# Performance work log

Hardware: AMD Instinct MI355X
Metric: run time of the kernel (lower is better)

The kernel has to match this reference:

```python
import jax, jax.numpy as jnp
import numpy as np

N_NODES = 100000
N_EDGES = 1600000
D_FEAT = 128
HIDDEN = 256


def setup_inputs() -> dict:
    key = jax.random.key(0)
    k1, k2, k3, k4, k5, k6, k7 = jax.random.split(key, 7)
    h = jax.random.normal(k1, (N_NODES, D_FEAT), dtype=jnp.float32)
    src = jax.random.randint(k2, (N_EDGES,), 0, N_NODES, dtype=jnp.int64)
    dst = jax.random.randint(k3, (N_EDGES,), 0, N_NODES, dtype=jnp.int64)
    # Linear weights, torch layout: W [out, in], b [out]
    lim1 = 1.0 / np.sqrt(2 * D_FEAT)
    W1_w = jax.random.uniform(k4, (HIDDEN, 2 * D_FEAT), minval=-lim1, maxval=lim1, dtype=jnp.float32)
    W1_b = jax.random.uniform(k5, (HIDDEN,), minval=-lim1, maxval=lim1, dtype=jnp.float32)
    lim2 = 1.0 / np.sqrt(HIDDEN)
    W2_w = jax.random.uniform(k6, (1, HIDDEN), minval=-lim2, maxval=lim2, dtype=jnp.float32)
    W2_b = jax.random.uniform(k7, (1,), minval=-lim2, maxval=lim2, dtype=jnp.float32)
    return {"h": h, "src": src, "dst": dst, "W1_w": W1_w, "W1_b": W1_b, "W2_w": W2_w, "W2_b": W2_b}


def reference(h, src, dst, W1_w, W1_b, W2_w, W2_b):
    # gather per-edge src/dst node features and concat: [E, 2D]
    x = jnp.concatenate([h[src], h[dst]], axis=1)
    # Linear -> ReLU -> Linear, squeeze last dim -> [E]
    hid = jax.nn.relu(x @ W1_w.T + W1_b)          # [E, H]
    score = (hid @ W2_w.T + W2_b)[:, 0]           # [E]
    return score
```

## Files before the change

kernel.cpp:

```cpp
#include <hip/hip_runtime.h>


#define NNODES 100000
#define E_TOTAL 1600000
#define D 128
#define K2 256
#define H 256

#define TILE_M 32
#define NTILES (E_TOTAL / TILE_M)
#define GRID 2500

typedef short bf16x8 __attribute__((ext_vector_type(8)));
typedef float f32x4 __attribute__((ext_vector_type(4)));
typedef const __attribute__((address_space(1))) unsigned short* gas_t;
typedef __attribute__((address_space(3))) unsigned short* las_t;

#if defined(__has_attribute)
#if __has_attribute(amdgpu_waves_per_eu)
#define LB __launch_bounds__(256) __attribute__((amdgpu_waves_per_eu(2, 2)))
#else
#define LB __launch_bounds__(256, 2)
#endif
#else
#define LB __launch_bounds__(256, 2)
#endif

__device__ __forceinline__ unsigned short f2bf(float f) {
    unsigned u = __float_as_uint(f);
    u += 0x7fff + ((u >> 16) & 1);
    return (unsigned short)(u >> 16);
}

__global__ void cvt_kernel(const float* __restrict__ h, const float* __restrict__ w1,
                           unsigned short* __restrict__ hbf, unsigned short* __restrict__ w1bf,
                           int n4h, int n4w) {
    int i = blockIdx.x * blockDim.x + threadIdx.x;
    const float* s; unsigned short* d; int j;
    if (i < n4h) { s = h; d = hbf; j = i; }
    else if (i < n4h + n4w) { s = w1; d = w1bf; j = i - n4h; }
    else return;
    float4 v = ((const float4*)s)[j];
    ushort4 o;
    o.x = f2bf(v.x); o.y = f2bf(v.y); o.z = f2bf(v.z); o.w = f2bf(v.w);
    ((ushort4*)d)[j] = o;
}

__global__ LB void edge_mlp(
    const unsigned short* __restrict__ hbf,
    const int* __restrict__ srcE,
    const int* __restrict__ dstE,
    const unsigned short* __restrict__ w1bf,
    const float* __restrict__ b1,
    const float* __restrict__ w2,
    const float* __restrict__ b2p,
    float* __restrict__ out)
{
    __shared__ __align__(16) unsigned short X[2][TILE_M * K2];
    __shared__ float red[2][TILE_M][5];

    const int tid = threadIdx.x;
    const int wave = tid >> 6;
    const int lane = tid & 63;
    const int lane15 = lane & 15;
    const int quad = lane >> 4;

    bf16x8 B[8][4];
#pragma unroll
    for (int kit = 0; kit < 8; ++kit) {
#pragma unroll
        for (int nt = 0; nt < 4; ++nt) {
            int n = wave * 64 + nt * 16 + lane15;
            int k = kit * 32 + quad * 8;
            B[kit][nt] = *(const bf16x8*)(w1bf + n * K2 + k);
        }
    }

    float b1v[4], w2v[4];
#pragma unroll
    for (int nt = 0; nt < 4; ++nt) {
        int n = wave * 64 + nt * 16 + lane15;
        b1v[nt] = b1[n];
        w2v[nt] = w2[n];
    }
    const float b2 = *b2p;

    const int r_off = tid >> 5;
    const int c = (tid & 31) ^ (r_off & 7);
    const int half = c >> 4;
    const int fc = c & 15;
    const int* idx_base = half ? dstE : srcE;
    const int gshort = fc * 8;

    const int t0 = blockIdx.x;
    int inode[4];

#pragma unroll
    for (int it = 0; it < 4; ++it)
        inode[it] = idx_base[t0 * TILE_M + it * 8 + r_off];
#pragma unroll
    for (int it = 0; it < 4; ++it)
        __builtin_amdgcn_global_load_lds(
            (gas_t)(hbf + inode[it] * D + gshort),
            (las_t)(&X[0][0] + it * 2048 + wave * 512), 16, 0, 0);
    {
        const int t1 = t0 + GRID;
#pragma unroll
        for (int it = 0; it < 4; ++it)
            inode[it] = idx_base[t1 * TILE_M + it * 8 + r_off];
    }

    int buf = 0;
    int prev_eb = -1;

    for (int tile = t0; tile < NTILES; tile += GRID) {
        __syncthreads();

        const int nt1 = tile + GRID;
        if (nt1 < NTILES) {
            unsigned short* Xn = &X[buf ^ 1][0];
#pragma unroll
            for (int it = 0; it < 4; ++it)
                __builtin_amdgcn_global_load_lds(
                    (gas_t)(hbf + inode[it] * D + gshort),
                    (las_t)(Xn + it * 2048 + wave * 512), 16, 0, 0);
        }
        const int nt2 = tile + 2 * GRID;
        if (nt2 < NTILES) {
            const int eb2 = nt2 * TILE_M;
#pragma unroll
            for (int it = 0; it < 4; ++it)
                inode[it] = idx_base[eb2 + it * 8 + r_off];
        }
        if (prev_eb >= 0 && tid < TILE_M) {
            float s = b2;
#pragma unroll
            for (int w = 0; w < 4; ++w) s += red[buf ^ 1][tid][w];
            out[prev_eb + tid] = s;
        }

        const unsigned short* Xc = &X[buf][0];
        f32x4 acc[2][4];
        const f32x4 zero = {0.f, 0.f, 0.f, 0.f};
#pragma unroll
        for (int ms = 0; ms < 2; ++ms)
#pragma unroll
            for (int nt = 0; nt < 4; ++nt)
                acc[ms][nt] = zero;

#pragma unroll
        for (int kit = 0; kit < 8; ++kit) {
            const int p8 = (((kit * 4 + quad) ^ (lane15 & 7))) * 8;
            bf16x8 a[2];
#pragma unroll
            for (int ms = 0; ms < 2; ++ms)
                a[ms] = *(const bf16x8*)&Xc[(ms * 16 + lane15) * K2 + p8];
#pragma unroll
            for (int ms = 0; ms < 2; ++ms)
#pragma unroll
                for (int nt = 0; nt < 4; ++nt)
                    acc[ms][nt] = __builtin_amdgcn_mfma_f32_16x16x32_bf16(
                        a[ms], B[kit][nt], acc[ms][nt], 0, 0, 0);
        }

#pragma unroll
        for (int ms = 0; ms < 2; ++ms) {
#pragma unroll
            for (int r = 0; r < 4; ++r) {
                float p = 0.f;
#pragma unroll
                for (int nt = 0; nt < 4; ++nt) {
                    float hv = acc[ms][nt][r] + b1v[nt];
                    p = fmaf(fmaxf(hv, 0.f), w2v[nt], p);
                }
                p += __shfl_xor(p, 1, 16);
                p += __shfl_xor(p, 2, 16);
                p += __shfl_xor(p, 4, 16);
                p += __shfl_xor(p, 8, 16);
                if (lane15 == 0) red[buf][ms * 16 + quad * 4 + r][wave] = p;
            }
        }
        prev_eb = tile * TILE_M;
        buf ^= 1;
    }

    __syncthreads();
    if (prev_eb >= 0 && tid < TILE_M) {
        float s = b2;
#pragma unroll
        for (int w = 0; w < 4; ++w) s += red[buf ^ 1][tid][w];
        out[prev_eb + tid] = s;
    }
}

extern "C" void kernel_launch(void* const* d_in, const int* in_sizes, int n_in,
                              void* d_out, int out_size, void* d_ws, size_t ws_size,
                              hipStream_t stream) {
    const float* h    = (const float*)d_in[0];
    const int*   srcE = (const int*)d_in[1];
    const int*   dstE = (const int*)d_in[2];
    const float* W1   = (const float*)d_in[3];
    const float* b1   = (const float*)d_in[4];
    const float* w2   = (const float*)d_in[5];
    const float* b2   = (const float*)d_in[6];
    float* out = (float*)d_out;

    unsigned short* hbf  = (unsigned short*)d_ws;
    unsigned short* w1bf = hbf + (size_t)NNODES * D;

    int n4h = NNODES * D / 4;
    int n4w = H * K2 / 4;
    int n4 = n4h + n4w;
    cvt_kernel<<<(n4 + 255) / 256, 256, 0, stream>>>(h, W1, hbf, w1bf, n4h, n4w);

    edge_mlp<<<GRID, 256, 0, stream>>>(hbf, srcE, dstE, w1bf, b1, w2, b2, out);
}
```

Before: 401.6 us.

## Precompute per-node W1 projections and reduce edge work to gather-add-relu-dot

Splits the first linear layer into separate source and destination halves and computes them per node with an MFMA GEMM into two bf16 planes, with bias folded into the source plane. A second kernel gathers the two 256-wide rows per edge, adds them, applies ReLU and dots with W2. This removes the per-edge GEMM but doubles the gathered bytes per edge and requires a larger workspace; it falls back to the old path if the workspace is too small. Rounding the projections to bf16 before the addition changes numerics slightly.

```diff
diff --git a/kernel.cpp b/kernel.cpp
--- a/kernel.cpp
+++ b/kernel.cpp
@@ -7,11 +7,8 @@
 #define K2 256
 #define H 256
 
-#define TILE_M 32
-#define NTILES (E_TOTAL / TILE_M)
-#define GRID 2500
-
 typedef short bf16x8 __attribute__((ext_vector_type(8)));
+typedef short bf16x4 __attribute__((ext_vector_type(4)));
 typedef float f32x4 __attribute__((ext_vector_type(4)));
 typedef const __attribute__((address_space(1))) unsigned short* gas_t;
 typedef __attribute__((address_space(3))) unsigned short* las_t;
@@ -31,6 +28,157 @@
     u += 0x7fff + ((u >> 16) & 1);
     return (unsigned short)(u >> 16);
 }
+__device__ __forceinline__ float bf2f(unsigned short s) {
+    return __uint_as_float((unsigned)s << 16);
+}
+
+
+__global__ LB void u_gemm(
+    const float* __restrict__ h,
+    const float* __restrict__ W1,
+    const float* __restrict__ b1,
+    unsigned short* __restrict__ Us,
+    unsigned short* __restrict__ Ud)
+{
+    __shared__ __align__(16) unsigned short A[64 * 136];
+
+    const int tid = threadIdx.x;
+    const int wave = tid >> 6;
+    const int lane = tid & 63;
+    const int l15 = lane & 15;
+    const int quad = lane >> 4;
+
+    const int r0 = blockIdx.x * 64;
+    int rows = NNODES - r0; if (rows > 64) rows = 64;
+
+    const float4* hf4 = (const float4*)(h + (size_t)r0 * D);
+    const int lim = rows * 32;
+#pragma unroll
+    for (int i = 0; i < 8; ++i) {
+        int j = tid + i * 256;
+        if (j < lim) {
+            float4 v = hf4[j];
+            bf16x4 b;
+            b[0] = (short)f2bf(v.x); b[1] = (short)f2bf(v.y);
+            b[2] = (short)f2bf(v.z); b[3] = (short)f2bf(v.w);
+            *(bf16x4*)&A[(j >> 5) * 136 + (j & 31) * 4] = b;
+        }
+    }
+    __syncthreads();
+
+#pragma unroll
+    for (int half = 0; half < 2; ++half) {
+        const int koff = half * 128;
+        unsigned short* U = half ? Ud : Us;
+
+        bf16x8 B[4][4];
+        float bias[4];
+#pragma unroll
+        for (int nt = 0; nt < 4; ++nt) {
+            const int n = wave * 64 + nt * 16 + l15;
+            bias[nt] = half ? 0.f : b1[n];
+#pragma unroll
+            for (int kit = 0; kit < 4; ++kit) {
+                const float* wp = W1 + (size_t)n * K2 + koff + kit * 32 + quad * 8;
+                float4 x = *(const float4*)wp;
+                float4 y = *(const float4*)(wp + 4);
+                bf16x8 f;
+                f[0] = (short)f2bf(x.x); f[1] = (short)f2bf(x.y);
+                f[2] = (short)f2bf(x.z); f[3] = (short)f2bf(x.w);
+                f[4] = (short)f2bf(y.x); f[5] = (short)f2bf(y.y);
+                f[6] = (short)f2bf(y.z); f[7] = (short)f2bf(y.w);
+                B[kit][nt] = f;
+            }
+        }
+
+        f32x4 acc[4][4];
+        const f32x4 zero = {0.f, 0.f, 0.f, 0.f};
+#pragma unroll
+        for (int ms = 0; ms < 4; ++ms)
+#pragma unroll
+            for (int nt = 0; nt < 4; ++nt)
+                acc[ms][nt] = zero;
+
+#pragma unroll
+        for (int kit = 0; kit < 4; ++kit) {
+            bf16x8 a[4];
+#pragma unroll
+            for (int ms = 0; ms < 4; ++ms)
+                a[ms] = *(const bf16x8*)&A[(ms * 16 + l15) * 136 + kit * 32 + quad * 8];
+#pragma unroll
+            for (int ms = 0; ms < 4; ++ms)
+#pragma unroll
+                for (int nt = 0; nt < 4; ++nt)
+                    acc[ms][nt] = __builtin_amdgcn_mfma_f32_16x16x32_bf16(
+                        a[ms], B[kit][nt], acc[ms][nt], 0, 0, 0);
+        }
+
+#pragma unroll
+        for (int ms = 0; ms < 4; ++ms) {
+#pragma unroll
+            for (int r = 0; r < 4; ++r) {
+                const int m = ms * 16 + quad * 4 + r;
+                if (m < rows) {
+                    unsigned short* rowp = U + (size_t)(r0 + m) * H + wave * 64;
+#pragma unroll
+                    for (int nt = 0; nt < 4; ++nt)
+                        rowp[nt * 16 + l15] = f2bf(acc[ms][nt][r] + bias[nt]);
+                }
+            }
+        }
+    }
+}
+
+__global__ __launch_bounds__(256) void edge_score(
+    const unsigned short* __restrict__ Us,
+    const unsigned short* __restrict__ Ud,
+    const int* __restrict__ srcE,
+    const int* __restrict__ dstE,
+    const float* __restrict__ w2,
+    const float* __restrict__ b2p,
+    float* __restrict__ out)
+{
+    const int gt = blockIdx.x * 256 + threadIdx.x;
+    const int l = gt & 15;
+    const int q = gt >> 4;
+    const int Q = (gridDim.x * 256) >> 4;
+
+    float w2v[16];
+#pragma unroll
+    for (int j = 0; j < 16; ++j) w2v[j] = w2[l * 16 + j];
+    const float b2 = *b2p;
+
+    for (int e = q; e < E_TOTAL; e += Q) {
+        const int s = srcE[e];
+        const int d = dstE[e];
+        const bf16x8* us = (const bf16x8*)(Us + (size_t)s * H + l * 16);
+        const bf16x8* ud = (const bf16x8*)(Ud + (size_t)d * H + l * 16);
+        bf16x8 u0 = us[0], u1 = us[1];
+        bf16x8 v0 = ud[0], v1 = ud[1];
+
+        float acc = 0.f;
+#pragma unroll
+        for (int j = 0; j < 8; ++j) {
+            float hv = bf2f((unsigned short)u0[j]) + bf2f((unsigned short)v0[j]);
+            acc = fmaf(fmaxf(hv, 0.f), w2v[j], acc);
+        }
+#pragma unroll
+        for (int j = 0; j < 8; ++j) {
+            float hv = bf2f((unsigned short)u1[j]) + bf2f((unsigned short)v1[j]);
+            acc = fmaf(fmaxf(hv, 0.f), w2v[j + 8], acc);
+        }
+        acc += __shfl_xor(acc, 1, 16);
+        acc += __shfl_xor(acc, 2, 16);
+        acc += __shfl_xor(acc, 4, 16);
+        acc += __shfl_xor(acc, 8, 16);
+        if (l == 0) out[e] = acc + b2;
+    }
+}
+
+
+#define TILE_M 32
+#define NTILES (E_TOTAL / TILE_M)
+#define GRID 2500
 
 __global__ void cvt_kernel(const float* __restrict__ h, const float* __restrict__ w1,
                            unsigned short* __restrict__ hbf, unsigned short* __restrict__ w1bf,
@@ -67,14 +215,13 @@
 
     bf16x8 B[8][4];
 #pragma unroll
-    for (int kit = 0; kit < 8; ++kit) {
+    for (int kit = 0; kit < 8; ++kit)
 #pragma unroll
         for (int nt = 0; nt < 4; ++nt) {
             int n = wave * 64 + nt * 16 + lane15;
             int k = kit * 32 + quad * 8;
             B[kit][nt] = *(const bf16x8*)(w1bf + n * K2 + k);
         }
-    }
 
     float b1v[4], w2v[4];
 #pragma unroll
@@ -164,7 +311,7 @@
         }
 
 #pragma unroll
-        for (int ms = 0; ms < 2; ++ms) {
+        for (int ms = 0; ms < 2; ++ms)
 #pragma unroll
             for (int r = 0; r < 4; ++r) {
                 float p = 0.f;
@@ -179,7 +326,6 @@
                 p += __shfl_xor(p, 8, 16);
                 if (lane15 == 0) red[buf][ms * 16 + quad * 4 + r][wave] = p;
             }
-        }
         prev_eb = tile * TILE_M;
         buf ^= 1;
     }
@@ -192,6 +338,7 @@
         out[prev_eb + tid] = s;
     }
 }
+
 
 extern "C" void kernel_launch(void* const* d_in, const int* in_sizes, int n_in,
                               void* d_out, int out_size, void* d_ws, size_t ws_size,
@@ -205,13 +352,21 @@
     const float* b2   = (const float*)d_in[6];
     float* out = (float*)d_out;
 
-    unsigned short* hbf  = (unsigned short*)d_ws;
-    unsigned short* w1bf = hbf + (size_t)NNODES * D;
-
-    int n4h = NNODES * D / 4;
-    int n4w = H * K2 / 4;
-    int n4 = n4h + n4w;
-    cvt_kernel<<<(n4 + 255) / 256, 256, 0, stream>>>(h, W1, hbf, w1bf, n4h, n4w);
-
-    edge_mlp<<<GRID, 256, 0, stream>>>(hbf, srcE, dstE, w1bf, b1, w2, b2, out);
-}
+    const size_t planeElems = (size_t)NNODES * H;
+    const size_t need = planeElems * 2 * sizeof(unsigned short);
+
+    if (ws_size >= need) {
+        unsigned short* Us = (unsigned short*)d_ws;
+        unsigned short* Ud = Us + planeElems;
+        u_gemm<<<(NNODES + 63) / 64, 256, 0, stream>>>(h, W1, b1, Us, Ud);
+        edge_score<<<4096, 256, 0, stream>>>(Us, Ud, srcE, dstE, w2, b2, out);
+    } else {
+        unsigned short* hbf  = (unsigned short*)d_ws;
+        unsigned short* w1bf = hbf + (size_t)NNODES * D;
+        int n4h = NNODES * D / 4;
+        int n4w = H * K2 / 4;
+        int n4 = n4h + n4w;
+        cvt_kernel<<<(n4 + 255) / 256, 256, 0, stream>>>(h, W1, hbf, w1bf, n4h, n4w);
+        edge_mlp<<<GRID, 256, 0, stream>>>(hbf, srcE, dstE, w1bf, b1, w2, b2, out);
+    }
+}
```

Result: no change. 394.5 us (-1.8%).
